# Optimization experiments

Measured on AMD Instinct MI355X. Metric: run time of the kernel, lower is better.

The kernel has to match this reference:

```python
import jax, jax.numpy as jnp
import numpy as np

B, N, F_IN, F_OUT = 64, 1024, 256, 64


def setup_inputs() -> dict:
    key = jax.random.key(0)
    k1, k2, k3, k4 = jax.random.split(key, 4)
    # xavier_uniform with gain=1.414 ~= sqrt(2): limit = gain*sqrt(6/(fan_in+fan_out))
    limW = 1.414 * np.sqrt(6.0 / (F_IN + F_OUT))
    lima = 1.414 * np.sqrt(6.0 / (2 * F_OUT + 1))
    return {
        "input": jax.random.normal(k1, (B, N, F_IN), dtype=jnp.float32),
        "adj": jax.random.randint(k2, (B, N, N), 0, 2, dtype=jnp.int32),
        "W": jax.random.uniform(k3, (F_IN, F_OUT), jnp.float32, -limW, limW),
        "a": jax.random.uniform(k4, (2 * F_OUT, 1), jnp.float32, -lima, lima),
    }


def reference(input, adj, W, a):
    # h = input @ W : (B, N, Fo)
    h = jnp.matmul(input, W)
    Bs, n, Fo = h.shape
    a1 = a[:Fo, 0]   # applied to the (scrambled) left block of a_input
    a2 = a[Fo:, 0]   # applied to the tiled right block

    # The original builds a_input by repeat_interleave(N, dim=2).view -> the left
    # block's row (i*N + j) holds h[b, i, (j*Fo + t)//N] for t in [0, Fo).
    # Its dot with a1 is therefore h[b, i, :] @ M[j, :] with
    #   M[j, f] = sum_{t : (j*Fo+t)//N == f} a1[t]
    idx = (jnp.arange(n)[:, None] * Fo + jnp.arange(Fo)[None, :]) // n  # (N, Fo), values in [0, Fo)
    rows = jnp.broadcast_to(jnp.arange(n)[:, None], (n, Fo))
    M = jnp.zeros((n, Fo), h.dtype).at[rows, idx].add(jnp.broadcast_to(a1, (n, Fo)))  # (N, Fo)

    e1 = jnp.einsum("bif,jf->bij", h, M)          # left-block contribution, (B, N, N)
    e2 = jnp.einsum("bjf,f->bj", h, a2)           # right block = h tiled over i, (B, N)
    # leakyrelu result is immediately overwritten by relu in the source; only relu matters
    e = jax.nn.relu(e1 + e2[:, None, :])

    neg = jnp.asarray(-9e15, e.dtype)
    attention = jax.nn.softmax(jnp.where(adj > 0, e, neg), axis=2)
    # F.dropout omitted (inference / deterministic reference)
    h_prime = jnp.matmul(attention, h)            # (B, N, Fo)
    return jax.nn.elu(h_prime)                    # concat=True branch
```

## Files before the change

kernel.cpp:

```cpp
#include <hip/hip_runtime.h>
#include <math.h>

#define B_   64
#define N_   1024
#define FIN_ 256
#define FO_  64

__global__ __launch_bounds__(256, 4) void k1_hproj(
    const float* __restrict__ input,
    const float* __restrict__ W,
    const float* __restrict__ a,
    float* __restrict__ h,
    float* __restrict__ e2)
{
    __shared__ float in_lds[64][65];
    __shared__ float W_lds[64][64];

    const int t   = threadIdx.x;
    const int tx  = t & 15;
    const int tyg = t >> 4;
    const int r0  = blockIdx.x * 64;

    float acc[4][4] = {};
    float4 ireg[4], wreg[4];

    auto load_chunk = [&](int k0) {
        #pragma unroll
        for (int it = 0; it < 4; ++it) {
            const int idx = it * 256 + t;
            const int row = idx >> 4;
            const int kq  = (idx & 15) * 4;
            ireg[it] = *reinterpret_cast<const float4*>(
                &input[(size_t)(r0 + row) * FIN_ + k0 + kq]);
            wreg[it] = *reinterpret_cast<const float4*>(
                &W[(size_t)(k0 + row) * FO_ + kq]);
        }
    };
    auto store_chunk = [&]() {
        #pragma unroll
        for (int it = 0; it < 4; ++it) {
            const int idx = it * 256 + t;
            const int row = idx >> 4;
            const int kq  = (idx & 15) * 4;
            in_lds[row][kq + 0] = ireg[it].x;
            in_lds[row][kq + 1] = ireg[it].y;
            in_lds[row][kq + 2] = ireg[it].z;
            in_lds[row][kq + 3] = ireg[it].w;
            *reinterpret_cast<float4*>(&W_lds[row][kq]) = wreg[it];
        }
    };

    load_chunk(0);
    #pragma unroll 1
    for (int c = 0; c < 4; ++c) {
        store_chunk();
        __syncthreads();
        if (c < 3) load_chunk((c + 1) * 64);
        #pragma unroll 4
        for (int k = 0; k < 64; ++k) {
            float af[4];
            #pragma unroll
            for (int mi = 0; mi < 4; ++mi) af[mi] = in_lds[tyg * 4 + mi][k];
            const float4 bf = *reinterpret_cast<const float4*>(&W_lds[k][tx * 4]);
            #pragma unroll
            for (int mi = 0; mi < 4; ++mi) {
                acc[mi][0] = fmaf(af[mi], bf.x, acc[mi][0]);
                acc[mi][1] = fmaf(af[mi], bf.y, acc[mi][1]);
                acc[mi][2] = fmaf(af[mi], bf.z, acc[mi][2]);
                acc[mi][3] = fmaf(af[mi], bf.w, acc[mi][3]);
            }
        }
        __syncthreads();
    }

    const float4 a2v = *reinterpret_cast<const float4*>(&a[FO_ + tx * 4]);
    #pragma unroll
    for (int mi = 0; mi < 4; ++mi) {
        const int row = r0 + tyg * 4 + mi;
        float4 hv;
        hv.x = acc[mi][0]; hv.y = acc[mi][1]; hv.z = acc[mi][2]; hv.w = acc[mi][3];
        *reinterpret_cast<float4*>(&h[(size_t)row * FO_ + tx * 4]) = hv;
        float p = acc[mi][0] * a2v.x + acc[mi][1] * a2v.y +
                  acc[mi][2] * a2v.z + acc[mi][3] * a2v.w;
        p += __shfl_xor(p, 1);
        p += __shfl_xor(p, 2);
        p += __shfl_xor(p, 4);
        p += __shfl_xor(p, 8);
        if (tx == 0) e2[row] = p;
    }
}

__global__ __launch_bounds__(256, 4) void k2_attn(
    const float* __restrict__ h,
    const int*   __restrict__ adj,
    const float* __restrict__ a,
    const float* __restrict__ e2,
    float* __restrict__ out)
{
    __shared__ float h_lds[2][32][64];
    __shared__ float wT[2][32][64];
    __shared__ float den_lds[64][4];

    const int t   = threadIdx.x;
    const int tx  = t & 15;
    const int tyg = t >> 4;
    const int b   = blockIdx.y;
    const int i0  = blockIdx.x * 64;

    const int wi  = t >> 2;
    const int ws  = t & 3;
    const int jl0 = ws * 8;

    const float* hb     = h + (size_t)b * N_ * FO_;
    const float* e2b    = e2 + (size_t)b * N_;
    const int*   adjrow = adj + ((size_t)b * N_ + i0 + wi) * N_;

    float S1 = 0.f;
    #pragma unroll
    for (int f = 0; f < FO_; f += 4) {
        const float4 av = *reinterpret_cast<const float4*>(&a[f]);
        S1 += av.x + av.y + av.z + av.w;
    }

    float acc[4][4] = {};
    float denreg = 0.f;

    int4   areg[2];
    float4 hreg[2];
    float4 e2reg[2];
    float2 c2reg;

    auto prefetch = [&](int tile) {
        const int jt = tile * 32;
        areg[0] = *reinterpret_cast<const int4*>(&adjrow[jt + jl0]);
        areg[1] = *reinterpret_cast<const int4*>(&adjrow[jt + jl0 + 4]);
        #pragma unroll
        for (int it = 0; it < 2; ++it) {
            const int idx = it * 256 + t;
            const int j = idx >> 4, fq = (idx & 15) * 4;
            hreg[it] = *reinterpret_cast<const float4*>(
                &hb[(size_t)(jt + j) * FO_ + fq]);
        }
        e2reg[0] = *reinterpret_cast<const float4*>(&e2b[jt + jl0]);
        e2reg[1] = *reinterpret_cast<const float4*>(&e2b[jt + jl0 + 4]);
        c2reg = *reinterpret_cast<const float2*>(
            &hb[(size_t)(i0 + wi) * FO_ + (jt >> 4)]);
    };

    auto phaseW = [&](int buf) {
        #pragma unroll
        for (int it = 0; it < 2; ++it) {
            const int idx = it * 256 + t;
            const int j = idx >> 4, fq = (idx & 15) * 4;
            *reinterpret_cast<float4*>(&h_lds[buf][j][fq]) = hreg[it];
        }
        const float cg = S1 * ((ws < 2) ? c2reg.x : c2reg.y);
        const int   aa[8] = { areg[0].x, areg[0].y, areg[0].z, areg[0].w,
                              areg[1].x, areg[1].y, areg[1].z, areg[1].w };
        const float ee[8] = { e2reg[0].x, e2reg[0].y, e2reg[0].z, e2reg[0].w,
                              e2reg[1].x, e2reg[1].y, e2reg[1].z, e2reg[1].w };
        #pragma unroll
        for (int dd = 0; dd < 8; ++dd) {
            const float ev = fmaxf(cg + ee[dd], 0.f);
            const float w  = aa[dd] ? __expf(ev) : 0.f;
            denreg += w;
            wT[buf][jl0 + dd][wi] = w;
        }
    };

    auto phaseG = [&](int buf) {
        #pragma unroll 8
        for (int jl = 0; jl < 32; ++jl) {
            const float4 wv = *reinterpret_cast<const float4*>(&wT[buf][jl][tyg * 4]);
            const float4 hv = *reinterpret_cast<const float4*>(&h_lds[buf][jl][tx * 4]);
            acc[0][0] = fmaf(wv.x, hv.x, acc[0][0]); acc[0][1] = fmaf(wv.x, hv.y, acc[0][1]);
            acc[0][2] = fmaf(wv.x, hv.z, acc[0][2]); acc[0][3] = fmaf(wv.x, hv.w, acc[0][3]);
            acc[1][0] = fmaf(wv.y, hv.x, acc[1][0]); acc[1][1] = fmaf(wv.y, hv.y, acc[1][1]);
            acc[1][2] = fmaf(wv.y, hv.z, acc[1][2]); acc[1][3] = fmaf(wv.y, hv.w, acc[1][3]);
            acc[2][0] = fmaf(wv.z, hv.x, acc[2][0]); acc[2][1] = fmaf(wv.z, hv.y, acc[2][1]);
            acc[2][2] = fmaf(wv.z, hv.z, acc[2][2]); acc[2][3] = fmaf(wv.z, hv.w, acc[2][3]);
            acc[3][0] = fmaf(wv.w, hv.x, acc[3][0]); acc[3][1] = fmaf(wv.w, hv.y, acc[3][1]);
            acc[3][2] = fmaf(wv.w, hv.z, acc[3][2]); acc[3][3] = fmaf(wv.w, hv.w, acc[3][3]);
        }
    };

    prefetch(0);
    phaseW(0);
    prefetch(1);
    __syncthreads();

    int cur = 0;
    #pragma unroll 1
    for (int tile = 0; tile < 32; ++tile) {
        if (tile < 31) phaseW(cur ^ 1);
        if (tile < 30) prefetch(tile + 2);
        phaseG(cur);
        __syncthreads();
        cur ^= 1;
    }

    den_lds[wi][ws] = denreg;
    __syncthreads();

    #pragma unroll
    for (int mi = 0; mi < 4; ++mi) {
        const int i = tyg * 4 + mi;
        const float4 dv = *reinterpret_cast<const float4*>(&den_lds[i][0]);
        const float inv = 1.0f / (dv.x + dv.y + dv.z + dv.w);
        float v[4];
        #pragma unroll
        for (int q = 0; q < 4; ++q) {
            const float x = acc[mi][q] * inv;
            v[q] = (x > 0.f) ? x : expm1f(x);
        }
        float4 o; o.x = v[0]; o.y = v[1]; o.z = v[2]; o.w = v[3];
        *reinterpret_cast<float4*>(
            &out[((size_t)b * N_ + i0 + i) * FO_ + tx * 4]) = o;
    }
}

extern "C" void kernel_launch(void* const* d_in, const int* in_sizes, int n_in,
                              void* d_out, int out_size, void* d_ws, size_t ws_size,
                              hipStream_t stream) {
    const float* input = (const float*)d_in[0];
    const int*   adj   = (const int*)d_in[1];
    const float* W     = (const float*)d_in[2];
    const float* a     = (const float*)d_in[3];
    float* out = (float*)d_out;

    float* h  = (float*)d_ws;
    float* e2 = (float*)((char*)d_ws + (size_t)B_ * N_ * FO_ * sizeof(float));

    k1_hproj<<<dim3((B_ * N_) / 64), dim3(256), 0, stream>>>(input, W, a, h, e2);
    k2_attn<<<dim3(N_ / 64, B_), dim3(256), 0, stream>>>(h, adj, a, e2, out);
}
```

Before: 531.2 us.

## Move both matmuls to bf16 split-precision MFMA with transposed h layout

```diff
diff --git a/kernel.cpp b/kernel.cpp
--- a/kernel.cpp
+++ b/kernel.cpp
@@ -6,47 +6,108 @@
 #define FIN_ 256
 #define FO_  64
 
+typedef __attribute__((ext_vector_type(4))) float f32x4;
+typedef __attribute__((ext_vector_type(8))) short short8;
+
+__device__ __forceinline__ unsigned short f2bf_rne(float f) {
+    union { float f; unsigned u; } v; v.f = f;
+    const unsigned r = v.u + 0x7fffu + ((v.u >> 16) & 1u);
+    return (unsigned short)(r >> 16);
+}
+__device__ __forceinline__ float bf2f(unsigned short h) {
+    union { unsigned u; float f; } v; v.u = ((unsigned)h) << 16;
+    return v.f;
+}
+
+__global__ void k0_wt(const float* __restrict__ W,
+                      unsigned short* __restrict__ WThi,
+                      unsigned short* __restrict__ WTlo)
+{
+    const int idx = blockIdx.x * 256 + threadIdx.x;
+    const int k = idx >> 6, f = idx & 63;
+    const float w = W[idx];
+    const unsigned short hi = f2bf_rne(w);
+    const unsigned short lo = f2bf_rne(w - bf2f(hi));
+    WThi[f * FIN_ + k] = hi;
+    WTlo[f * FIN_ + k] = lo;
+}
+
 __global__ __launch_bounds__(256, 4) void k1_hproj(
     const float* __restrict__ input,
-    const float* __restrict__ W,
+    const unsigned short* __restrict__ WThi,
+    const unsigned short* __restrict__ WTlo,
     const float* __restrict__ a,
-    float* __restrict__ h,
+    unsigned short* __restrict__ hbT,
+    unsigned short* __restrict__ hrT,
     float* __restrict__ e2)
 {
-    __shared__ float in_lds[64][65];
-    __shared__ float W_lds[64][64];
-
-    const int t   = threadIdx.x;
-    const int tx  = t & 15;
-    const int tyg = t >> 4;
-    const int r0  = blockIdx.x * 64;
-
-    float acc[4][4] = {};
-    float4 ireg[4], wreg[4];
-
-    auto load_chunk = [&](int k0) {
-        #pragma unroll
-        for (int it = 0; it < 4; ++it) {
-            const int idx = it * 256 + t;
-            const int row = idx >> 4;
-            const int kq  = (idx & 15) * 4;
-            ireg[it] = *reinterpret_cast<const float4*>(
-                &input[(size_t)(r0 + row) * FIN_ + k0 + kq]);
-            wreg[it] = *reinterpret_cast<const float4*>(
-                &W[(size_t)(k0 + row) * FO_ + kq]);
+    __shared__ union {
+        struct { unsigned short Ahi[64*64], Alo[64*64], Bhi[64*64], Blo[64*64]; } s;
+        struct { unsigned short hb[64*72], hr[64*72]; } e;
+    } u;
+
+    const int t  = threadIdx.x;
+    const int r0 = blockIdx.x * 64;
+    const int b  = blockIdx.x >> 4;
+    const int jb = r0 & (N_ - 1);
+
+    const int l = t & 63, lm = l & 15, lk = l >> 4, wm0 = (t >> 6) * 16;
+
+    f32x4 acc[4] = {};
+    float4 iv[2][2];
+    short8 wh[2], wl[2];
+
+    auto load_chunk = [&](int c0) {
+        #pragma unroll
+        for (int q = 0; q < 2; ++q) {
+            const int ci = t * 2 + q;
+            const int row = ci >> 3, cc = ci & 7;
+            iv[q][0] = *reinterpret_cast<const float4*>(
+                &input[(size_t)(r0 + row) * FIN_ + c0 + cc * 8]);
+            iv[q][1] = *reinterpret_cast<const float4*>(
+                &input[(size_t)(r0 + row) * FIN_ + c0 + cc * 8 + 4]);
+            wh[q] = *reinterpret_cast<const short8*>(&WThi[row * FIN_ + c0 + cc * 8]);
+            wl[q] = *reinterpret_cast<const short8*>(&WTlo[row * FIN_ + c0 + cc * 8]);
         }
     };
     auto store_chunk = [&]() {
         #pragma unroll
-        for (int it = 0; it < 4; ++it) {
-            const int idx = it * 256 + t;
-            const int row = idx >> 4;
-            const int kq  = (idx & 15) * 4;
-            in_lds[row][kq + 0] = ireg[it].x;
-            in_lds[row][kq + 1] = ireg[it].y;
-            in_lds[row][kq + 2] = ireg[it].z;
-            in_lds[row][kq + 3] = ireg[it].w;
-            *reinterpret_cast<float4*>(&W_lds[row][kq]) = wreg[it];
+        for (int q = 0; q < 2; ++q) {
+            const int ci = t * 2 + q;
+            const int row = ci >> 3, cc = ci & 7;
+            const int pos = (cc ^ (row & 7)) * 8;
+            alignas(16) float xv[8];
+            *reinterpret_cast<float4*>(&xv[0]) = iv[q][0];
+            *reinterpret_cast<float4*>(&xv[4]) = iv[q][1];
+            alignas(16) unsigned short h8[8], l8[8];
+            #pragma unroll
+            for (int e = 0; e < 8; ++e) {
+                h8[e] = f2bf_rne(xv[e]);
+                l8[e] = f2bf_rne(xv[e] - bf2f(h8[e]));
+            }
+            *reinterpret_cast<short8*>(&u.s.Ahi[row * 64 + pos]) = *reinterpret_cast<short8*>(h8);
+            *reinterpret_cast<short8*>(&u.s.Alo[row * 64 + pos]) = *reinterpret_cast<short8*>(l8);
+            *reinterpret_cast<short8*>(&u.s.Bhi[row * 64 + pos]) = wh[q];
+            *reinterpret_cast<short8*>(&u.s.Blo[row * 64 + pos]) = wl[q];
+        }
+    };
+    auto compute = [&]() {
+        #pragma unroll
+        for (int ks = 0; ks < 2; ++ks) {
+            const int mrow = wm0 + lm;
+            const int ac = (((ks << 2) + lk) ^ (mrow & 7)) * 8;
+            const short8 ah = *reinterpret_cast<const short8*>(&u.s.Ahi[mrow * 64 + ac]);
+            const short8 al = *reinterpret_cast<const short8*>(&u.s.Alo[mrow * 64 + ac]);
+            #pragma unroll
+            for (int nt = 0; nt < 4; ++nt) {
+                const int fr = nt * 16 + lm;
+                const int bc = (((ks << 2) + lk) ^ (fr & 7)) * 8;
+                const short8 bh = *reinterpret_cast<const short8*>(&u.s.Bhi[fr * 64 + bc]);
+                const short8 bl = *reinterpret_cast<const short8*>(&u.s.Blo[fr * 64 + bc]);
+                acc[nt] = __builtin_amdgcn_mfma_f32_16x16x32_bf16(ah, bh, acc[nt], 0, 0, 0);
+                acc[nt] = __builtin_amdgcn_mfma_f32_16x16x32_bf16(ah, bl, acc[nt], 0, 0, 0);
+                acc[nt] = __builtin_amdgcn_mfma_f32_16x16x32_bf16(al, bh, acc[nt], 0, 0, 0);
+            }
         }
     };
 
@@ -56,64 +117,73 @@
         store_chunk();
         __syncthreads();
         if (c < 3) load_chunk((c + 1) * 64);
-        #pragma unroll 4
-        for (int k = 0; k < 64; ++k) {
-            float af[4];
-            #pragma unroll
-            for (int mi = 0; mi < 4; ++mi) af[mi] = in_lds[tyg * 4 + mi][k];
-            const float4 bf = *reinterpret_cast<const float4*>(&W_lds[k][tx * 4]);
-            #pragma unroll
-            for (int mi = 0; mi < 4; ++mi) {
-                acc[mi][0] = fmaf(af[mi], bf.x, acc[mi][0]);
-                acc[mi][1] = fmaf(af[mi], bf.y, acc[mi][1]);
-                acc[mi][2] = fmaf(af[mi], bf.z, acc[mi][2]);
-                acc[mi][3] = fmaf(af[mi], bf.w, acc[mi][3]);
-            }
-        }
+        compute();
         __syncthreads();
     }
 
-    const float4 a2v = *reinterpret_cast<const float4*>(&a[FO_ + tx * 4]);
+    float ap[4];
     #pragma unroll
-    for (int mi = 0; mi < 4; ++mi) {
-        const int row = r0 + tyg * 4 + mi;
-        float4 hv;
-        hv.x = acc[mi][0]; hv.y = acc[mi][1]; hv.z = acc[mi][2]; hv.w = acc[mi][3];
-        *reinterpret_cast<float4*>(&h[(size_t)row * FO_ + tx * 4]) = hv;
-        float p = acc[mi][0] * a2v.x + acc[mi][1] * a2v.y +
-                  acc[mi][2] * a2v.z + acc[mi][3] * a2v.w;
-        p += __shfl_xor(p, 1);
-        p += __shfl_xor(p, 2);
-        p += __shfl_xor(p, 4);
-        p += __shfl_xor(p, 8);
-        if (tx == 0) e2[row] = p;
+    for (int nt = 0; nt < 4; ++nt) ap[nt] = a[FO_ + nt * 16 + lm];
+
+    #pragma unroll
+    for (int reg = 0; reg < 4; ++reg) {
+        const int row = wm0 + lk * 4 + reg;
+        float e2p = 0.f;
+        #pragma unroll
+        for (int nt = 0; nt < 4; ++nt) {
+            const float hv = acc[nt][reg];
+            e2p += hv * ap[nt];
+            const unsigned short hh = f2bf_rne(hv);
+            const unsigned short hr = f2bf_rne(hv - bf2f(hh));
+            const int f = nt * 16 + lm;
+            u.e.hb[f * 72 + row] = hh;
+            u.e.hr[f * 72 + row] = hr;
+        }
+        e2p += __shfl_xor(e2p, 1);
+        e2p += __shfl_xor(e2p, 2);
+        e2p += __shfl_xor(e2p, 4);
+        e2p += __shfl_xor(e2p, 8);
+        if (lm == 0) e2[r0 + row] = e2p;
+    }
+    __syncthreads();
+
+    {
+        const int f = t >> 2, seg = t & 3;
+        const size_t gb = ((size_t)(b * FO_ + f)) * N_ + jb + seg * 16;
+        *reinterpret_cast<short8*>(&hbT[gb]) =
+            *reinterpret_cast<const short8*>(&u.e.hb[f * 72 + seg * 16]);
+        *reinterpret_cast<short8*>(&hbT[gb + 8]) =
+            *reinterpret_cast<const short8*>(&u.e.hb[f * 72 + seg * 16 + 8]);
+        *reinterpret_cast<short8*>(&hrT[gb]) =
+            *reinterpret_cast<const short8*>(&u.e.hr[f * 72 + seg * 16]);
+        *reinterpret_cast<short8*>(&hrT[gb + 8]) =
+            *reinterpret_cast<const short8*>(&u.e.hr[f * 72 + seg * 16 + 8]);
     }
 }
 
 __global__ __launch_bounds__(256, 4) void k2_attn(
-    const float* __restrict__ h,
+    const unsigned short* __restrict__ hbT,
+    const unsigned short* __restrict__ hrT,
     const int*   __restrict__ adj,
     const float* __restrict__ a,
     const float* __restrict__ e2,
     float* __restrict__ out)
 {
-    __shared__ float h_lds[2][32][64];
-    __shared__ float wT[2][32][64];
+    __shared__ unsigned short whi_lds[2][64*32], wlo_lds[2][64*32];
+    __shared__ unsigned short hb_lds [2][64*32], hr_lds [2][64*32];
     __shared__ float den_lds[64][4];
 
-    const int t   = threadIdx.x;
-    const int tx  = t & 15;
-    const int tyg = t >> 4;
-    const int b   = blockIdx.y;
-    const int i0  = blockIdx.x * 64;
-
-    const int wi  = t >> 2;
-    const int ws  = t & 3;
-    const int jl0 = ws * 8;
-
-    const float* hb     = h + (size_t)b * N_ * FO_;
+    const int t  = threadIdx.x;
+    const int b  = blockIdx.y;
+    const int i0 = blockIdx.x * 64;
+
+    const int wi = t >> 2, ws = t & 3, jl0 = ws * 8;
+    const int l = t & 63, lm = l & 15, lk = l >> 4, wm0 = (t >> 6) * 16;
+
+    const int*   adjrow = adj + ((size_t)b * N_ + i0 + wi) * N_;
     const float* e2b    = e2 + (size_t)b * N_;
-    const int*   adjrow = adj + ((size_t)b * N_ + i0 + wi) * N_;
+    const unsigned short* hbTb = hbT + (size_t)b * FO_ * N_;
+    const unsigned short* hrTb = hrT + (size_t)b * FO_ * N_;
 
     float S1 = 0.f;
     #pragma unroll
@@ -122,65 +192,60 @@
         S1 += av.x + av.y + av.z + av.w;
     }
 
-    float acc[4][4] = {};
+    f32x4 acc[4] = {};
     float denreg = 0.f;
 
     int4   areg[2];
-    float4 hreg[2];
-    float4 e2reg[2];
-    float2 c2reg;
+    short8 hbreg, hrreg;
+    float4 e2r[2];
+    float  c2r;
 
     auto prefetch = [&](int tile) {
         const int jt = tile * 32;
         areg[0] = *reinterpret_cast<const int4*>(&adjrow[jt + jl0]);
         areg[1] = *reinterpret_cast<const int4*>(&adjrow[jt + jl0 + 4]);
-        #pragma unroll
-        for (int it = 0; it < 2; ++it) {
-            const int idx = it * 256 + t;
-            const int j = idx >> 4, fq = (idx & 15) * 4;
-            hreg[it] = *reinterpret_cast<const float4*>(
-                &hb[(size_t)(jt + j) * FO_ + fq]);
-        }
-        e2reg[0] = *reinterpret_cast<const float4*>(&e2b[jt + jl0]);
-        e2reg[1] = *reinterpret_cast<const float4*>(&e2b[jt + jl0 + 4]);
-        c2reg = *reinterpret_cast<const float2*>(
-            &hb[(size_t)(i0 + wi) * FO_ + (jt >> 4)]);
+        hbreg = *reinterpret_cast<const short8*>(&hbTb[(size_t)wi * N_ + jt + ws * 8]);
+        hrreg = *reinterpret_cast<const short8*>(&hrTb[(size_t)wi * N_ + jt + ws * 8]);
+        e2r[0] = *reinterpret_cast<const float4*>(&e2b[jt + jl0]);
+        e2r[1] = *reinterpret_cast<const float4*>(&e2b[jt + jl0 + 4]);
+        const int g = (jt >> 4) + (ws >> 1);
+        c2r = bf2f(hbTb[(size_t)g * N_ + i0 + wi]) + bf2f(hrTb[(size_t)g * N_ + i0 + wi]);
     };
 
     auto phaseW = [&](int buf) {
-        #pragma unroll
-        for (int it = 0; it < 2; ++it) {
-            const int idx = it * 256 + t;
-            const int j = idx >> 4, fq = (idx & 15) * 4;
-            *reinterpret_cast<float4*>(&h_lds[buf][j][fq]) = hreg[it];
-        }
-        const float cg = S1 * ((ws < 2) ? c2reg.x : c2reg.y);
-        const int   aa[8] = { areg[0].x, areg[0].y, areg[0].z, areg[0].w,
-                              areg[1].x, areg[1].y, areg[1].z, areg[1].w };
-        const float ee[8] = { e2reg[0].x, e2reg[0].y, e2reg[0].z, e2reg[0].w,
-                              e2reg[1].x, e2reg[1].y, e2reg[1].z, e2reg[1].w };
-        #pragma unroll
-        for (int dd = 0; dd < 8; ++dd) {
-            const float ev = fmaxf(cg + ee[dd], 0.f);
-            const float w  = aa[dd] ? __expf(ev) : 0.f;
-            denreg += w;
-            wT[buf][jl0 + dd][wi] = w;
-        }
+        *reinterpret_cast<short8*>(&hb_lds[buf][wi * 32 + ws * 8]) = hbreg;
+        *reinterpret_cast<short8*>(&hr_lds[buf][wi * 32 + ws * 8]) = hrreg;
+        const float cg = S1 * c2r;
+        const int aa[8] = { areg[0].x, areg[0].y, areg[0].z, areg[0].w,
+                            areg[1].x, areg[1].y, areg[1].z, areg[1].w };
+        alignas(16) float ee[8];
+        *reinterpret_cast<float4*>(&ee[0]) = e2r[0];
+        *reinterpret_cast<float4*>(&ee[4]) = e2r[1];
+        alignas(16) unsigned short w_hi[8], w_lo[8];
+        #pragma unroll
+        for (int d = 0; d < 8; ++d) {
+            const float ev = fmaxf(cg + ee[d], 0.f);
+            const float w  = aa[d] ? __expf(ev) : 0.f;
+            const unsigned short hi = f2bf_rne(w);
+            const unsigned short lo = f2bf_rne(w - bf2f(hi));
+            w_hi[d] = hi; w_lo[d] = lo;
+            denreg += bf2f(hi) + bf2f(lo);
+        }
+        *reinterpret_cast<short8*>(&whi_lds[buf][wi * 32 + jl0]) = *reinterpret_cast<short8*>(w_hi);
+        *reinterpret_cast<short8*>(&wlo_lds[buf][wi * 32 + jl0]) = *reinterpret_cast<short8*>(w_lo);
     };
 
     auto phaseG = [&](int buf) {
-        #pragma unroll 8
-        for (int jl = 0; jl < 32; ++jl) {
-            const float4 wv = *reinterpret_cast<const float4*>(&wT[buf][jl][tyg * 4]);
-            const float4 hv = *reinterpret_cast<const float4*>(&h_lds[buf][jl][tx * 4]);
-            acc[0][0] = fmaf(wv.x, hv.x, acc[0][0]); acc[0][1] = fmaf(wv.x, hv.y, acc[0][1]);
-            acc[0][2] = fmaf(wv.x, hv.z, acc[0][2]); acc[0][3] = fmaf(wv.x, hv.w, acc[0][3]);
-            acc[1][0] = fmaf(wv.y, hv.x, acc[1][0]); acc[1][1] = fmaf(wv.y, hv.y, acc[1][1]);
-            acc[1][2] = fmaf(wv.y, hv.z, acc[1][2]); acc[1][3] = fmaf(wv.y, hv.w, acc[1][3]);
-            acc[2][0] = fmaf(wv.z, hv.x, acc[2][0]); acc[2][1] = fmaf(wv.z, hv.y, acc[2][1]);
-            acc[2][2] = fmaf(wv.z, hv.z, acc[2][2]); acc[2][3] = fmaf(wv.z, hv.w, acc[2][3]);
-            acc[3][0] = fmaf(wv.w, hv.x, acc[3][0]); acc[3][1] = fmaf(wv.w, hv.y, acc[3][1]);
-            acc[3][2] = fmaf(wv.w, hv.z, acc[3][2]); acc[3][3] = fmaf(wv.w, hv.w, acc[3][3]);
+        const short8 awh = *reinterpret_cast<const short8*>(&whi_lds[buf][(wm0 + lm) * 32 + lk * 8]);
+        const short8 awl = *reinterpret_cast<const short8*>(&wlo_lds[buf][(wm0 + lm) * 32 + lk * 8]);
+        #pragma unroll
+        for (int nt = 0; nt < 4; ++nt) {
+            const int fr = nt * 16 + lm;
+            const short8 bh = *reinterpret_cast<const short8*>(&hb_lds[buf][fr * 32 + lk * 8]);
+            const short8 br = *reinterpret_cast<const short8*>(&hr_lds[buf][fr * 32 + lk * 8]);
+            acc[nt] = __builtin_amdgcn_mfma_f32_16x16x32_bf16(awh, bh, acc[nt], 0, 0, 0);
+            acc[nt] = __builtin_amdgcn_mfma_f32_16x16x32_bf16(awh, br, acc[nt], 0, 0, 0);
+            acc[nt] = __builtin_amdgcn_mfma_f32_16x16x32_bf16(awl, bh, acc[nt], 0, 0, 0);
         }
     };
 
@@ -203,19 +268,16 @@
     __syncthreads();
 
     #pragma unroll
-    for (int mi = 0; mi < 4; ++mi) {
-        const int i = tyg * 4 + mi;
+    for (int reg = 0; reg < 4; ++reg) {
+        const int i = wm0 + lk * 4 + reg;
         const float4 dv = *reinterpret_cast<const float4*>(&den_lds[i][0]);
         const float inv = 1.0f / (dv.x + dv.y + dv.z + dv.w);
-        float v[4];
-        #pragma unroll
-        for (int q = 0; q < 4; ++q) {
-            const float x = acc[mi][q] * inv;
-            v[q] = (x > 0.f) ? x : expm1f(x);
-        }
-        float4 o; o.x = v[0]; o.y = v[1]; o.z = v[2]; o.w = v[3];
-        *reinterpret_cast<float4*>(
-            &out[((size_t)b * N_ + i0 + i) * FO_ + tx * 4]) = o;
+        #pragma unroll
+        for (int nt = 0; nt < 4; ++nt) {
+            const float x = acc[nt][reg] * inv;
+            const float y = (x > 0.f) ? x : expm1f(x);
+            out[((size_t)b * N_ + i0 + i) * FO_ + nt * 16 + lm] = y;
+        }
     }
 }
 
@@ -228,9 +290,14 @@
     const float* a     = (const float*)d_in[3];
     float* out = (float*)d_out;
 
-    float* h  = (float*)d_ws;
-    float* e2 = (float*)((char*)d_ws + (size_t)B_ * N_ * FO_ * sizeof(float));
-
-    k1_hproj<<<dim3((B_ * N_) / 64), dim3(256), 0, stream>>>(input, W, a, h, e2);
-    k2_attn<<<dim3(N_ / 64, B_), dim3(256), 0, stream>>>(h, adj, a, e2, out);
-}
+    char* ws = (char*)d_ws;
+    unsigned short* hbT  = (unsigned short*)(ws);
+    unsigned short* hrT  = (unsigned short*)(ws + (8u << 20));
+    float*          e2   = (float*)(ws + (16u << 20));
+    unsigned short* WThi = (unsigned short*)(ws + (16u << 20) + (256u << 10));
+    unsigned short* WTlo = WThi + FO_ * FIN_;
+
+    k0_wt  <<<dim3(64),                 dim3(256), 0, stream>>>(W, WThi, WTlo);
+    k1_hproj<<<dim3((B_ * N_) / 64),    dim3(256), 0, stream>>>(input, WThi, WTlo, a, hbT, hrT, e2);
+    k2_attn<<<dim3(N_ / 64, B_),        dim3(256), 0, stream>>>(hbT, hrT, adj, a, e2, out);
+}
```

After: 442.2 us. -16.8%, faster.
